# Kernel optimization log

Hardware: AMD Instinct MI355X
Metric: run time of the kernel (lower is better)

Reference implementation:

```python
import jax, jax.numpy as jnp
import numpy as np
jax.config.update("jax_enable_x64", True)

BASE = [2654435761, 2246822519, 3266489917, 2028178513, 1220703125, 1610612741, 805306457, 402653189,
        3674653429, 2860486313, 1073676287, 2971215073, 1500450271, 3267000013, 2654435789, 4049292737]
EXT32 = BASE + [2246822531, 3266489927, 2028178519, 1220703133, 1610612759, 805306463, 402653201, 3674653441,
                2860486319, 1073676311, 2971215091, 1500450277, 3267000023, 2654435801, 4049292751, 2246822537]
HASH_PRIMES = [
    BASE[:1], BASE[:2], BASE[:4], BASE[:8], BASE[:16],
    [p ^ 3735928559 for p in EXT32],
    [p ^ 3405691582 for p in (BASE[:8] * 8)],
    [p ^ 2343432205 for p in (BASE[:8] * 16)],
]
SCALE_WINDOWS = [1, 2, 4, 8, 16, 32, 64, 128]
BUCKETS = 65536
NUM_SCALES = 8
E = 16
BOUNDARY = 4
SIGN_BITS = 8
COND_PRIMES = BASE[:SIGN_BITS]


def _hash_scale(tokens, scale_idx):
    # tokens: [B, T] int64. Rolling polynomial hash over a window of past tokens.
    T = tokens.shape[1]
    primes = HASH_PRIMES[scale_idx][:SCALE_WINDOWS[scale_idx]]
    h = jnp.zeros_like(tokens)
    for i, p in enumerate(primes):
        off = i + 1
        if off >= T:
            continue
        shifted = jnp.pad(tokens[:, :-off], ((0, 0), (off, 0)))  # shift right by off
        h = h ^ (shifted * p)
    return h % BUCKETS


def setup_inputs() -> dict:
    key = jax.random.key(0)
    k1, k2, k3 = jax.random.split(key, 3)
    B, T = 32, 4096
    tokens = jax.random.randint(k1, (B, T), 0, 1024, dtype=jnp.int64)
    tables = (0.02 * jax.random.normal(k2, (NUM_SCALES, BUCKETS, E))).astype(jnp.float32)
    Wc = (0.02 * jax.random.normal(k3, (SIGN_BITS, BOUNDARY * E))).astype(jnp.float32)
    return {"tokens": tokens, "tables": tables, "Wc": Wc}


def reference(tokens, tables, Wc):
    keys = [_hash_scale(tokens, s) for s in range(NUM_SCALES)]  # each [B, T] int64 in [0, BUCKETS)
    # short-range scale embeddings
    short = [tables[s][keys[s]] for s in range(BOUNDARY)]  # each [B, T, E]
    short_cat = jnp.concatenate(short, axis=-1)            # [B, T, BOUNDARY*E]
    cond_logits = short_cat @ Wc.T                         # [B, T, SIGN_BITS]
    sign_bits = (cond_logits > 0).astype(jnp.int64)
    cond_key = jnp.zeros(tokens.shape, dtype=jnp.int64)
    for i in range(SIGN_BITS):
        cond_key = cond_key ^ (sign_bits[:, :, i] * COND_PRIMES[i])
    long = [tables[s][(keys[s] ^ cond_key) % BUCKETS] for s in range(BOUNDARY, NUM_SCALES)]
    return jnp.stack(short + long, axis=2)  # [B, T, NUM_SCALES, E]
```

## Files before the change

### kernel.cpp

```cpp
#include <hip/hip_runtime.h>

typedef unsigned int u32;

__device__ constexpr u32 BASEP[16] = {
    2654435761u, 2246822519u, 3266489917u, 2028178513u,
    1220703125u, 1610612741u,  805306457u,  402653189u,
    3674653429u, 2860486313u, 1073676287u, 2971215073u,
    1500450271u, 3267000013u, 2654435789u, 4049292737u};
__device__ constexpr u32 EXTP[16] = {
    2246822531u, 3266489927u, 2028178519u, 1220703133u,
    1610612759u,  805306463u,  402653201u, 3674653441u,
    2860486319u, 1073676311u, 2971215091u, 1500450277u,
    3267000023u, 2654435801u, 4049292751u, 2246822537u};

#define TDIM 4096
#define PPB  64
#define HALO 128
#define NTOK (HALO + PPB)

__device__ __forceinline__ int dpp_x1(int x) {
    return __builtin_amdgcn_update_dpp(0, x, 0xB1, 0xF, 0xF, true);
}
__device__ __forceinline__ int dpp_x2(int x) {
    return __builtin_amdgcn_update_dpp(0, x, 0x4E, 0xF, 0xF, true);
}
__device__ __forceinline__ int dpp_x4(int x) {
    int y = __builtin_amdgcn_update_dpp(0, x, 0x104, 0xF, 0x5, false);
    return  __builtin_amdgcn_update_dpp(y, x, 0x114, 0xF, 0xA, false);
}
__device__ __forceinline__ int dpp_x8(int x) {
    return __builtin_amdgcn_update_dpp(0, x, 0x128, 0xF, 0xF, true);
}
__device__ __forceinline__ u32 bxor16(u32 x) {
    x ^= (u32)dpp_x1((int)x);
    x ^= (u32)dpp_x2((int)x);
    x ^= (u32)dpp_x4((int)x);
    x ^= (u32)dpp_x8((int)x);
    return x;
}
__device__ __forceinline__ float fsum16(float x) {
    x += __int_as_float(dpp_x1(__float_as_int(x)));
    x += __int_as_float(dpp_x2(__float_as_int(x)));
    x += __int_as_float(dpp_x4(__float_as_int(x)));
    x += __int_as_float(dpp_x8(__float_as_int(x)));
    return x;
}

__global__ __launch_bounds__(256) void rhp_fused(
        const int* __restrict__ tokens, const float* __restrict__ tables,
        const float* __restrict__ Wc, float* __restrict__ out)
{
    __shared__ u32   toks[NTOK];
    __shared__ float wc_s[512];
    __shared__ u32   bp16[16], ep16[16];

    const int tid = threadIdx.x;
    const int g0  = blockIdx.x * PPB;
    const int t0  = g0 & (TDIM - 1);

    if (tid < 16) { bp16[tid] = BASEP[tid] & 0xFFFFu;
                    ep16[tid] = EXTP[tid]  & 0xFFFFu; }
    if (tid < 128) ((float4*)wc_s)[tid] = ((const float4*)Wc)[tid];
    if (tid < NTOK) {
        const int t = t0 - HALO + tid;
        toks[tid] = (t >= 0) ? (u32)tokens[g0 - HALO + tid] : 0u;
    }
    __syncthreads();

    const int r    = tid & 15;
    const int slot = tid >> 4;
    const int s    = (tid >> 2) & 3;
    const int q    = tid & 3;

    float4 w[8];
#pragma unroll
    for (int j = 0; j < 8; ++j) w[j] = ((const float4*)wc_s)[j * 16 + s * 4 + q];

    const u32 pb  = bp16[r];
    const u32 pb7 = bp16[r & 7];
    const u32 pe  = ep16[r];
    const u32 p7  = pb7 ^ 0xF00Du;
    const u32 p6  = pb7 ^ 0xBABEu;
    const u32 p5a = pb  ^ 0xBEEFu;
    const u32 p5b = pe  ^ 0xBEEFu;

    const int base = HALO - 1 + slot - r;
    u32 v0 = toks[base      ], v1 = toks[base -  16];
    u32 v2 = toks[base -  32], v3 = toks[base -  48];
    u32 v4 = toks[base -  64], v5 = toks[base -  80];
    u32 v6 = toks[base -  96], v7 = toks[base - 112];

    const float* tshort = tables + (u32)s * 1048576u + (u32)q * 4u;
    const float* tlong  = tshort + 4u * 1048576u;
    float* o = out + (size_t)(g0 + slot) * 128u + (u32)s * 16u + (u32)q * 4u;

#pragma unroll
    for (int it = 0; it < 4; ++it) {
        u32 k7 = __umul24(v0, p7) ^ __umul24(v1, p7) ^ __umul24(v2, p7) ^
                 __umul24(v3, p7) ^ __umul24(v4, p7) ^ __umul24(v5, p7) ^
                 __umul24(v6, p7) ^ __umul24(v7, p7);
        u32 k6 = __umul24(v0, p6) ^ __umul24(v1, p6) ^
                 __umul24(v2, p6) ^ __umul24(v3, p6);
        u32 k5 = __umul24(v0, p5a) ^ __umul24(v1, p5b);
        u32 k4 = __umul24(v0, pb);
        const u32 k3 = (r < 8) ? k4 : 0u;
        const u32 k2 = (r < 4) ? k4 : 0u;
        const u32 k1 = (r < 2) ? k4 : 0u;
        const u32 k0 = (r == 0) ? k4 : 0u;

        u32 P0 = (k0 & 0xFFFFu) | ((k4 & 0xFFFFu) << 16);
        u32 P1 = (k1 & 0xFFFFu) | ((k5 & 0xFFFFu) << 16);
        u32 P2 = (k2 & 0xFFFFu) | ((k6 & 0xFFFFu) << 16);
        u32 P3 = (k3 & 0xFFFFu) | ((k7 & 0xFFFFu) << 16);
        P0 = bxor16(P0); P1 = bxor16(P1); P2 = bxor16(P2); P3 = bxor16(P3);

        const u32 Ps = (s == 0) ? P0 : (s == 1) ? P1 : (s == 2) ? P2 : P3;
        const u32 ks = Ps & 0xFFFFu;

        const float4 sv = *(const float4*)(tshort + ks * 16u);
        *(float4*)o = sv;

        float lg[8];
#pragma unroll
        for (int j = 0; j < 8; ++j)
            lg[j] = fmaf(sv.x, w[j].x, fmaf(sv.y, w[j].y,
                     fmaf(sv.z, w[j].z, sv.w * w[j].w)));
#pragma unroll
        for (int j = 0; j < 8; ++j) lg[j] = fsum16(lg[j]);

        u32 ck = 0u;
#pragma unroll
        for (int j = 0; j < 8; ++j)
            if (lg[j] > 0.0f) ck ^= (BASEP[j] & 0xFFFFu);

        const u32 kl = ((Ps >> 16) ^ ck) & 0xFFFFu;
        const float4 lv = *(const float4*)(tlong + kl * 16u);
        *(float4*)(o + 64u) = lv;

        if (it < 3) {
            v7 = v6; v6 = v5; v5 = v4; v4 = v3;
            v3 = v2; v2 = v1; v1 = v0;
            v0 = toks[base + 16 * (it + 1)];
            o += 16 * 128;
        }
    }
}

extern "C" void kernel_launch(void* const* d_in, const int* in_sizes, int n_in,
                              void* d_out, int out_size, void* d_ws, size_t ws_size,
                              hipStream_t stream) {
    const int*   tokens = (const int*)d_in[0];
    const float* tables = (const float*)d_in[1];
    const float* Wc     = (const float*)d_in[2];
    float*       out    = (float*)d_out;

    const int n_pos = in_sizes[0];
    hipLaunchKernelGGL(rhp_fused, dim3(n_pos / PPB), dim3(256), 0, stream,
                       tokens, tables, Wc, out);
}
```

Before: 109.3 us.

## Batch table gathers across iterations and use nontemporal output stores

Hash keys for all four positions are computed first. The four short-table gathers are then issued together so their latencies overlap, followed by the four dependent long-table gathers, and output stores are deferred and batched. Output writes now use nontemporal stores so the streaming output does not pollute cache. This raises register pressure by holding more float4 values live at once.

Measured after the change: 107.9 us. No clear change (-1.3%).

```diff
diff --git a/kernel.cpp b/kernel.cpp
--- a/kernel.cpp
+++ b/kernel.cpp
@@ -1,6 +1,7 @@
 #include <hip/hip_runtime.h>
 
 typedef unsigned int u32;
+typedef float f4 __attribute__((ext_vector_type(4)));
 
 __device__ constexpr u32 BASEP[16] = {
     2654435761u, 2246822519u, 3266489917u, 2028178513u,
@@ -90,10 +91,7 @@
     u32 v4 = toks[base -  64], v5 = toks[base -  80];
     u32 v6 = toks[base -  96], v7 = toks[base - 112];
 
-    const float* tshort = tables + (u32)s * 1048576u + (u32)q * 4u;
-    const float* tlong  = tshort + 4u * 1048576u;
-    float* o = out + (size_t)(g0 + slot) * 128u + (u32)s * 16u + (u32)q * 4u;
-
+    u32 Pk[4];
 #pragma unroll
     for (int it = 0; it < 4; ++it) {
         u32 k7 = __umul24(v0, p7) ^ __umul24(v1, p7) ^ __umul24(v2, p7) ^
@@ -113,18 +111,32 @@
         u32 P2 = (k2 & 0xFFFFu) | ((k6 & 0xFFFFu) << 16);
         u32 P3 = (k3 & 0xFFFFu) | ((k7 & 0xFFFFu) << 16);
         P0 = bxor16(P0); P1 = bxor16(P1); P2 = bxor16(P2); P3 = bxor16(P3);
+        Pk[it] = (s == 0) ? P0 : (s == 1) ? P1 : (s == 2) ? P2 : P3;
 
-        const u32 Ps = (s == 0) ? P0 : (s == 1) ? P1 : (s == 2) ? P2 : P3;
-        const u32 ks = Ps & 0xFFFFu;
+        if (it < 3) {
+            v7 = v6; v6 = v5; v5 = v4; v4 = v3;
+            v3 = v2; v2 = v1; v1 = v0;
+            v0 = toks[base + 16 * (it + 1)];
+        }
+    }
 
-        const float4 sv = *(const float4*)(tshort + ks * 16u);
-        *(float4*)o = sv;
+    const float* tshort = tables + (u32)s * 1048576u + (u32)q * 4u;
+    const float* tlong  = tshort + 4u * 1048576u;
+    float* o = out + (size_t)(g0 + slot) * 128u + (u32)s * 16u + (u32)q * 4u;
 
+    float4 sv[4];
+#pragma unroll
+    for (int it = 0; it < 4; ++it)
+        sv[it] = *(const float4*)(tshort + (Pk[it] & 0xFFFFu) * 16u);
+
+    float4 lv[4];
+#pragma unroll
+    for (int it = 0; it < 4; ++it) {
         float lg[8];
 #pragma unroll
         for (int j = 0; j < 8; ++j)
-            lg[j] = fmaf(sv.x, w[j].x, fmaf(sv.y, w[j].y,
-                     fmaf(sv.z, w[j].z, sv.w * w[j].w)));
+            lg[j] = fmaf(sv[it].x, w[j].x, fmaf(sv[it].y, w[j].y,
+                     fmaf(sv[it].z, w[j].z, sv[it].w * w[j].w)));
 #pragma unroll
         for (int j = 0; j < 8; ++j) lg[j] = fsum16(lg[j]);
 
@@ -133,17 +145,17 @@
         for (int j = 0; j < 8; ++j)
             if (lg[j] > 0.0f) ck ^= (BASEP[j] & 0xFFFFu);
 
-        const u32 kl = ((Ps >> 16) ^ ck) & 0xFFFFu;
-        const float4 lv = *(const float4*)(tlong + kl * 16u);
-        *(float4*)(o + 64u) = lv;
+        const u32 kl = ((Pk[it] >> 16) ^ ck) & 0xFFFFu;
+        lv[it] = *(const float4*)(tlong + kl * 16u);
 
-        if (it < 3) {
-            v7 = v6; v6 = v5; v5 = v4; v4 = v3;
-            v3 = v2; v2 = v1; v1 = v0;
-            v0 = toks[base + 16 * (it + 1)];
-            o += 16 * 128;
-        }
+        __builtin_nontemporal_store((f4){sv[it].x, sv[it].y, sv[it].z, sv[it].w},
+                                    (f4*)(o + it * 2048));
     }
+
+#pragma unroll
+    for (int it = 0; it < 4; ++it)
+        __builtin_nontemporal_store((f4){lv[it].x, lv[it].y, lv[it].z, lv[it].w},
+                                    (f4*)(o + it * 2048 + 64));
 }
 
 extern "C" void kernel_launch(void* const* d_in, const int* in_sizes, int n_in,
```
